# Performance work log

Hardware: AMD Instinct MI355X
Metric: run time of the kernel (lower is better)

## Reference

```python
import jax, jax.numpy as jnp
import numpy as np

B, NB, BS, C, H = 4, 128, 128, 256, 8  # batch, num_blocks, block_size, dim, heads


def setup_inputs() -> dict:
    key = jax.random.key(0)
    ks = jax.random.split(key, 8)
    x = jax.random.normal(ks[0], (B, NB * BS, C), dtype=jnp.float32)
    attn_mask = jax.random.randint(ks[1], (NB, BS, BS + 1), 0, 2, dtype=jnp.int32)
    # guarantee the global-node column is always attendable (avoids all--inf rows)
    attn_mask = attn_mask.at[:, :, BS].set(1)
    edge_feats = jax.random.normal(ks[2], (NB, BS, BS + 1, 4), dtype=jnp.float32)
    w_qkv = jax.random.normal(ks[3], (C, 3 * C), dtype=jnp.float32) * (C ** -0.5)
    b_qkv = jnp.zeros((3 * C,), dtype=jnp.float32)
    w_proj = jax.random.normal(ks[4], (C, C), dtype=jnp.float32) * (C ** -0.5)
    b_proj = jnp.zeros((C,), dtype=jnp.float32)
    w_gate = jax.random.normal(ks[5], (4, H), dtype=jnp.float32) * 0.01  # nn.init.normal_(std=0.01)
    b_gate = jnp.zeros((H,), dtype=jnp.float32)
    return {"x": x, "attn_mask": attn_mask, "edge_feats": edge_feats,
            "w_qkv": w_qkv, "b_qkv": b_qkv, "w_proj": w_proj, "b_proj": b_proj,
            "w_gate": w_gate, "b_gate": b_gate}


def reference(x, attn_mask, edge_feats, w_qkv, b_qkv, w_proj, b_proj, w_gate, b_gate):
    Bv, N, Cv = x.shape
    nb, bs, _ = attn_mask.shape
    Hv = b_gate.shape[0]
    hd = Cv // Hv
    scale = hd ** -0.5

    x_blk = x.reshape(Bv, nb, bs, Cv)
    block_node = x_blk.mean(axis=2, keepdims=True)           # [B, nb, 1, C]
    kv = jnp.concatenate([x_blk, block_node], axis=2)        # [B, nb, bs+1, C]

    qkv_q = x_blk @ w_qkv + b_qkv
    qkv_kv = kv @ w_qkv + b_qkv
    q = qkv_q[..., :Cv].reshape(Bv, nb, bs, Hv, hd)
    k = qkv_kv[..., Cv:2 * Cv].reshape(Bv, nb, bs + 1, Hv, hd)
    v = qkv_kv[..., 2 * Cv:].reshape(Bv, nb, bs + 1, Hv, hd)

    scores = jnp.einsum('bnqhd,bnkhd->bnqkh', q, k) * scale  # [B, nb, bs, bs+1, H]

    # physics bias: zero out (with channel-3 = 1) at the global-node column and the diagonal
    qi = jnp.arange(bs)[:, None]
    ki = jnp.arange(bs + 1)[None, :]
    special = (ki == bs) | (ki == qi)                        # [bs, bs+1]
    special_vec = jnp.array([0.0, 0.0, 0.0, 1.0], dtype=x.dtype)
    bias = jnp.where(special[:, :, None], special_vec, edge_feats[..., :4])  # [nb, bs, bs+1, 4]
    bias = jnp.broadcast_to(bias[None], (Bv, nb, bs, bs + 1, 4))

    scores = scores + bias[..., 3:4]
    mask = (attn_mask[None, :, :, :, None] != 0)             # [1, nb, bs, bs+1, 1]
    scores = jnp.where(mask, scores, -jnp.inf)
    probs = jax.nn.softmax(scores, axis=3)

    gate = jnp.where(mask, bias @ w_gate + b_gate, jnp.zeros((), dtype=x.dtype))
    combined = probs + gate                                  # [B, nb, bs, bs+1, H]

    out = jnp.einsum('bnqkh,bnkhd->bnqhd', combined, v).reshape(Bv, N, Cv)
    return out @ w_proj + b_proj
```

## Files before the change

### kernel.cpp

```cpp
#include <hip/hip_runtime.h>

#define B_   4
#define NB_  128
#define BS_  128
#define C_   256
#define H_   8
#define KL_  129
#define SC2_   0.25503486f
#define LOG2E_ 1.4426950408889634f
#define LN2_   0.6931471805599453f
#define RSTR_  99072

typedef unsigned short u16;
typedef unsigned int   u32;
typedef short          s16;
typedef __attribute__((ext_vector_type(8))) __bf16 bf16x8;
typedef __attribute__((ext_vector_type(4))) float  f32x4;

__device__ __forceinline__ float bf16tof(u16 u) {
  union { u32 i; float f; } v; v.i = ((u32)u) << 16; return v.f;
}
__device__ __forceinline__ u16 ftobf16(float f) {
  union { float f; u32 i; } v; v.f = f;
  u32 b = v.i + 0x7FFFu + ((v.i >> 16) & 1u);
  return (u16)(b >> 16);
}
__device__ __forceinline__ u32 pk2(float a, float b) {
  return (u32)ftobf16(a) | ((u32)ftobf16(b) << 16);
}
__device__ __forceinline__ float asf(u32 u) {
  union { u32 i; float f; } v; v.i = u; return v.f;
}

__device__ __forceinline__ void glds16(const void* g, void* l) {
  __builtin_amdgcn_global_load_lds(
      (const __attribute__((address_space(1))) unsigned int*)g,
      (__attribute__((address_space(3))) unsigned int*)l, 16, 0, 0);
}

__global__ __launch_bounds__(256) void meancvt_kernel(const float* __restrict__ x,
                                                      u16* __restrict__ xb) {
  const int blk = blockIdx.x;
  const int c = threadIdx.x;
  const float* p = x + (size_t)blk * BS_ * C_ + c;
  u16* q = xb + (size_t)blk * (KL_ * C_) + c;
  float s = 0.f;
  #pragma unroll 4
  for (int r = 0; r < BS_; ++r) {
    const float v = p[(size_t)r * C_];
    s += v;
    q[(size_t)r * C_] = ftobf16(v);
  }
  q[(size_t)BS_ * C_] = ftobf16(s * (1.0f / BS_));
}

__global__ __launch_bounds__(256) void wt_kernel(const float* __restrict__ wq,
      const float* __restrict__ wp, s16* __restrict__ wtq, s16* __restrict__ wtp) {
  const int i = blockIdx.x * 256 + threadIdx.x;
  if (i < 768 * 256) {
    const int nn = i >> 8, k = i & 255;
    wtq[i] = (s16)ftobf16(wq[k * 768 + nn]);
  } else {
    const int j = i - 768 * 256;
    const int nn = j >> 8, k = j & 255;
    wtp[j] = (s16)ftobf16(wp[k * 256 + nn]);
  }
}

__global__ __launch_bounds__(256) void pre_kernel(const int* __restrict__ mask,
      const float* __restrict__ ef, u16* __restrict__ e4t) {
  const int t = blockIdx.x * 256 + threadIdx.x;
  const int kq = t & 31;
  const int row = t >> 5;
  const int q = row & 127;
  const int key0 = kq * 4;
  const int* mrow = mask + (size_t)row * KL_;
  const float* erow = ef + (size_t)row * KL_ * 4;
  u32 o[8];
  #pragma unroll
  for (int r = 0; r < 4; ++r) {
    const int key = key0 + r;
    const int m = mrow[key];
    float4 e = *(const float4*)(erow + (size_t)key * 4);
    if (key == q) { e.x = 0.f; e.y = 0.f; e.z = 0.f; e.w = 1.f; }
    float e3L = e.w * LOG2E_;
    if (!m) { e.x = 0.f; e.y = 0.f; e.z = 0.f; e3L = -1e30f; }
    o[2*r]   = (u32)ftobf16(e.x) | ((u32)ftobf16(e.y) << 16);
    o[2*r+1] = (u32)ftobf16(e.z) | ((u32)ftobf16(e3L) << 16);
  }
  uint4* dst = (uint4*)(e4t + (size_t)row * 512 + key0 * 4);
  dst[0] = uint4{o[0], o[1], o[2], o[3]};
  dst[1] = uint4{o[4], o[5], o[6], o[7]};
}

template<bool STRIDED, bool OBF16, int NS>
__global__ __launch_bounds__(256) void mfma_gemm(const s16* __restrict__ Ab,
      const s16* __restrict__ Bt, const float* __restrict__ bias,
      void* __restrict__ outv) {
  __shared__ __align__(16) s16 Al[2][128 * 64];
  __shared__ __align__(16) s16 Bl[2][128 * 64];
  const int tid = threadIdx.x;
  const int lane = tid & 63;
  const int wid = tid >> 6;
  const int row0 = blockIdx.y * 128;
  const int col0 = blockIdx.x * 128;
  const int ldrow = lane >> 3;
  const int lcb   = (lane & 7) * 16;

  auto STAGE = [&](int k0, int buf) {
    #pragma unroll
    for (int j = 0; j < 4; ++j) {
      const int c = wid * 4 + j;
      const int row = c * 8 + ldrow;
      const int scb = lcb ^ ((row & 7) << 4);
      glds16(Bt + (size_t)(col0 + row) * C_ + k0 + (scb >> 1), &Bl[buf][c * 512]);
    }
    #pragma unroll
    for (int j = 0; j < 4; ++j) {
      const int c = wid * 4 + j;
      const int row = c * 8 + ldrow;
      const int scb = lcb ^ ((row & 7) << 4);
      if constexpr (STRIDED)
        glds16(Ab + (size_t)blockIdx.y * RSTR_ + (size_t)row * 768 + 256
                  + k0 + (scb >> 1), &Al[buf][c * 512]);
      else
        glds16(Ab + (size_t)(row0 + row) * C_ + k0 + (scb >> 1), &Al[buf][c * 512]);
    }
  };

  f32x4 acc[4][4];
  #pragma unroll
  for (int i = 0; i < 4; ++i)
    #pragma unroll
    for (int j = 0; j < 4; ++j) acc[i][j] = f32x4{0.f, 0.f, 0.f, 0.f};

  STAGE(0, 0);
  __syncthreads();

  const int fr = lane & 15;
  const int ar0 = (wid >> 1) * 64;
  const int ac0 = (wid & 1) * 64;
  #pragma unroll 1
  for (int t = 0; t < 4; ++t) {
    if (t < 3) STAGE((t + 1) * 64, (t + 1) & 1);
    const char* Ac = (const char*)&Al[t & 1][0];
    const char* Bc = (const char*)&Bl[t & 1][0];
    #pragma unroll
    for (int kk = 0; kk < 64; kk += 32) {
      const int kb = kk * 2 + (lane >> 4) * 16;
      bf16x8 af[4], bfr[4];
      #pragma unroll
      for (int mf = 0; mf < 4; ++mf) {
        const int row = ar0 + mf * 16 + fr;
        af[mf] = *(const bf16x8*)(Ac + row * 128 + (kb ^ ((row & 7) << 4)));
      }
      #pragma unroll
      for (int nf = 0; nf < 4; ++nf) {
        const int row = ac0 + nf * 16 + fr;
        bfr[nf] = *(const bf16x8*)(Bc + row * 128 + (kb ^ ((row & 7) << 4)));
      }
      #pragma unroll
      for (int mf = 0; mf < 4; ++mf)
        #pragma unroll
        for (int nf = 0; nf < 4; ++nf)
          acc[mf][nf] = __builtin_amdgcn_mfma_f32_16x16x32_bf16(
              af[mf], bfr[nf], acc[mf][nf], 0, 0, 0);
    }
    __syncthreads();
  }

  const int orow0 = row0 + (wid >> 1) * 64 + (lane >> 4) * 4;
  const int ocol0 = col0 + (wid & 1) * 64 + (lane & 15);
  #pragma unroll
  for (int nf = 0; nf < 4; ++nf) {
    const int col = ocol0 + nf * 16;
    const float bb = bias[col];
    #pragma unroll
    for (int mf = 0; mf < 4; ++mf) {
      #pragma unroll
      for (int r = 0; r < 4; ++r) {
        const size_t row = (size_t)(orow0 + mf * 16 + r);
        const float v = acc[mf][nf][r] + bb;
        if constexpr (OBF16) ((u16*)outv)[row * NS + col] = ftobf16(v);
        else                 ((float*)outv)[row * NS + col] = v;
      }
    }
  }
}

__global__ __launch_bounds__(256, 4) void attn_kernel(u16* __restrict__ qkv,
      const u16* __restrict__ e4t, const float* __restrict__ wg_,
      const float* __restrict__ bg) {
  __shared__ __align__(16) char lds[36176];
  const int bid = blockIdx.x;
  const int xcd = bid & 7;
  const int j   = bid >> 3;
  const int wgi = xcd * 64 + (j >> 3);
  const int h   = j & 7;
  const int n = wgi & (NB_ - 1);
  const int tid = threadIdx.x;
  const int wid = tid >> 6, lane = tid & 63;
  const int g = lane >> 4, ql = lane & 15;
  u16*  Kl = (u16*)lds;
  u16*  vt = (u16*)(lds + 10320);
  char* pb = lds + 18768 + wid * 4352;

  u16* qkv_blk = qkv + (size_t)wgi * RSTR_;
  const u16* ebase = e4t + (size_t)n * (128 * 512);

  for (int i = tid; i < 516; i += 256) {
    const int r = i >> 2, dc = i & 3;
    const uint4 u = *(const uint4*)(qkv_blk + (size_t)r * 768 + 256 + h * 32 + dc * 8);
    *(uint4*)(Kl + r * 40 + dc * 8) = u;
  }
  for (int i = tid; i < 512; i += 256) {
    const int r = i >> 2, dc = i & 3;
    const uint4 u = *(const uint4*)(qkv_blk + (size_t)r * 768 + 512 + h * 32 + dc * 8);
    u16* col = vt + (dc * 8) * 132 + r;
    col[0 * 132] = (u16)(u.x & 0xffff); col[1 * 132] = (u16)(u.x >> 16);
    col[2 * 132] = (u16)(u.y & 0xffff); col[3 * 132] = (u16)(u.y >> 16);
    col[4 * 132] = (u16)(u.z & 0xffff); col[5 * 132] = (u16)(u.z >> 16);
    col[6 * 132] = (u16)(u.w & 0xffff); col[7 * 132] = (u16)(u.w >> 16);
  }
  __syncthreads();

  const float v128a = bf16tof(qkv_blk[(size_t)128 * 768 + 512 + h * 32 + ql]);
  const float v128b = bf16tof(qkv_blk[(size_t)128 * 768 + 512 + h * 32 + 16 + ql]);

  const float wgc0 = wg_[h], wgc1 = wg_[8 + h], wgc2 = wg_[16 + h];
  const float wgc3s = wg_[24 + h] * LN2_;
  const float bgh = bg[h];
  const float gk128 = wg_[24 + h] + bgh;

  #pragma unroll 1
  for (int mi = 0; mi < 2; ++mi) {
    const int mt = wid * 2 + mi;
    const int qrow = mt * 16 + ql;
    const bf16x8 qf = *(const bf16x8*)(qkv_blk + (size_t)qrow * 768 + h * 32 + g * 8);
    const uint4* eql = (const uint4*)(ebase + (size_t)qrow * 512) + 2 * g;

    float psum = 0.f;
    uint2 gab[8];
    #pragma unroll
    for (int f = 0; f < 8; ++f) {
      const bf16x8 kf = *(const bf16x8*)(Kl + (16 * f + ql) * 40 + 8 * g);
      f32x4 st = __builtin_amdgcn_mfma_f32_16x16x32_bf16(
          kf, qf, f32x4{0.f, 0.f, 0.f, 0.f}, 0, 0, 0);
      const uint4 ea = eql[8 * f];
      const uint4 eb = eql[8 * f + 1];
      const u32 wa[4] = {ea.x, ea.z, eb.x, eb.z};
      const u32 wb[4] = {ea.y, ea.w, eb.y, eb.w};
      float w[4], gt[4];
      #pragma unroll
      for (int r = 0; r < 4; ++r) {
        const float e0 = asf(wa[r] << 16), e1 = asf(wa[r] & 0xffff0000u);
        const float e2 = asf(wb[r] << 16), e3L = asf(wb[r] & 0xffff0000u);
        const float gg = fmaf(e0, wgc0, fmaf(e1, wgc1,
                          fmaf(e2, wgc2, fmaf(e3L, wgc3s, bgh))));
        gt[r] = (e3L > -1e29f) ? gg : 0.f;
        w[r] = __builtin_amdgcn_exp2f(fmaf(st[r], SC2_, e3L));
        psum += w[r];
      }
      gab[f] = uint2{pk2(gt[0], gt[1]), pk2(gt[2], gt[3])};
      *(uint2*)(pb + ql * 272 + (16 * f + 4 * g) * 2) =
          uint2{pk2(w[0], w[1]), pk2(w[2], w[3])};
    }
    const bf16x8 kf8 = *(const bf16x8*)(Kl + 128 * 40 + 8 * g);
    f32x4 st8 = __builtin_amdgcn_mfma_f32_16x16x32_bf16(
        kf8, qf, f32x4{0.f, 0.f, 0.f, 0.f}, 0, 0, 0);
    const float w0 = __builtin_amdgcn_exp2f(
        fmaf(st8[0], SC2_, (g == 0) ? LOG2E_ : -1e30f));
    psum += w0;
    psum += __shfl_xor(psum, 16);
    psum += __shfl_xor(psum, 32);
    const float inv = __builtin_amdgcn_rcpf(psum);
    const float c128 = fmaf(w0, inv, (g == 0) ? gk128 : 0.f);

    f32x4 ow0{0.f,0.f,0.f,0.f}, ow1{0.f,0.f,0.f,0.f};
    #pragma unroll
    for (int c = 0; c < 4; ++c) {
      const bf16x8 pa = *(const bf16x8*)(pb + ql * 272 + (32 * c + 8 * g) * 2);
      const bf16x8 v0 = *(const bf16x8*)(vt + ql * 132 + 32 * c + 8 * g);
      const bf16x8 v1 = *(const bf16x8*)(vt + (16 + ql) * 132 + 32 * c + 8 * g);
      ow0 = __builtin_amdgcn_mfma_f32_16x16x32_bf16(pa, v0, ow0, 0, 0, 0);
      ow1 = __builtin_amdgcn_mfma_f32_16x16x32_bf16(pa, v1, ow1, 0, 0, 0);
    }
    #pragma unroll
    for (int f = 0; f < 8; ++f)
      *(uint2*)(pb + ql * 272 + (16 * f + 4 * g) * 2) = gab[f];
    f32x4 og0{0.f,0.f,0.f,0.f}, og1{0.f,0.f,0.f,0.f};
    #pragma unroll
    for (int c = 0; c < 4; ++c) {
      const bf16x8 pa = *(const bf16x8*)(pb + ql * 272 + (32 * c + 8 * g) * 2);
      const bf16x8 v0 = *(const bf16x8*)(vt + ql * 132 + 32 * c + 8 * g);
      const bf16x8 v1 = *(const bf16x8*)(vt + (16 + ql) * 132 + 32 * c + 8 * g);
      og0 = __builtin_amdgcn_mfma_f32_16x16x32_bf16(pa, v0, og0, 0, 0, 0);
      og1 = __builtin_amdgcn_mfma_f32_16x16x32_bf16(pa, v1, og1, 0, 0, 0);
    }
    u16* aop = qkv_blk + (size_t)(mt * 16 + g * 4) * 768 + 256 + h * 32 + ql;
    #pragma unroll
    for (int r = 0; r < 4; ++r) {
      const float iv = __shfl(inv,  4 * g + r);
      const float cc = __shfl(c128, 4 * g + r);
      aop[(size_t)r * 768]      = ftobf16(fmaf(cc, v128a, fmaf(ow0[r], iv, og0[r])));
      aop[(size_t)r * 768 + 16] = ftobf16(fmaf(cc, v128b, fmaf(ow1[r], iv, og1[r])));
    }
  }
}

extern "C" void kernel_launch(void* const* d_in, const int* in_sizes, int n_in,
                              void* d_out, int out_size, void* d_ws, size_t ws_size,
                              hipStream_t stream) {
  (void)in_sizes; (void)n_in; (void)out_size; (void)ws_size;
  const float* x      = (const float*)d_in[0];
  const int*   mask   = (const int*)  d_in[1];
  const float* ef     = (const float*)d_in[2];
  const float* w_qkv  = (const float*)d_in[3];
  const float* b_qkv  = (const float*)d_in[4];
  const float* w_proj = (const float*)d_in[5];
  const float* b_proj = (const float*)d_in[6];
  const float* w_gate = (const float*)d_in[7];
  const float* b_gate = (const float*)d_in[8];
  float* out = (float*)d_out;
  char* ws = (char*)d_ws;

  u16* qkv = (u16*)(ws);
  s16* wtq = (s16*)(ws + 101449728);
  s16* wtp = (s16*)(ws + 101842944);
  u16* xb  = (u16*)(ws + 101974016);
  u16* e4t = (u16*)(ws + 101974016);

  meancvt_kernel<<<B_ * NB_, 256, 0, stream>>>(x, xb);
  wt_kernel<<<(768 * 256 + 256 * 256) / 256, 256, 0, stream>>>(
      w_qkv, w_proj, wtq, wtp);
  mfma_gemm<false, true, 768>
      <<<dim3(6, (B_ * NB_ * KL_) / 128), 256, 0, stream>>>(
      (const s16*)xb, wtq, b_qkv, qkv);
  pre_kernel<<<(NB_ * BS_ * 32) / 256, 256, 0, stream>>>(mask, ef, e4t);
  attn_kernel<<<B_ * NB_ * H_, 256, 0, stream>>>(
      qkv, (const u16*)e4t, w_gate, b_gate);
  mfma_gemm<true, false, 256>
      <<<dim3(2, (B_ * NB_ * BS_) / 128), 256, 0, stream>>>(
      (const s16*)qkv, wtp, b_proj, out);
}
```

Baseline: 213.0 us.

## Remap GEMM tiles per XCD and use hardware bf16 conversion

The two MFMA GEMMs now launch on a 1D grid, and block indices are remapped so that consecutive tiles sharing the same A rows land on the same XCD (blockIdx & 7 selects a contiguous chunk). This is meant to improve L2 reuse of A and B tiles across the chiplets. Separately, the manual round-to-nearest-even bf16 conversion is replaced with the compiler's __bf16 cast, which may lower to native conversion instructions and cut ALU work. The compiler cast may round NaNs or edge cases slightly differently from the hand-written version.

```diff
diff --git a/kernel.cpp b/kernel.cpp
--- a/kernel.cpp
+++ b/kernel.cpp
@@ -20,13 +20,13 @@
 __device__ __forceinline__ float bf16tof(u16 u) {
   union { u32 i; float f; } v; v.i = ((u32)u) << 16; return v.f;
 }
-__device__ __forceinline__ u16 ftobf16(float f) {
-  union { float f; u32 i; } v; v.f = f;
-  u32 b = v.i + 0x7FFFu + ((v.i >> 16) & 1u);
-  return (u16)(b >> 16);
+__device__ __forceinline__ u16 fbits(float a) {
+  union { __bf16 h; u16 u; } v; v.h = (__bf16)a; return v.u;
 }
 __device__ __forceinline__ u32 pk2(float a, float b) {
-  return (u32)ftobf16(a) | ((u32)ftobf16(b) << 16);
+  union { __bf16 h[2]; u32 u; } v;
+  v.h[0] = (__bf16)a; v.h[1] = (__bf16)b;
+  return v.u;
 }
 __device__ __forceinline__ float asf(u32 u) {
   union { u32 i; float f; } v; v.i = u; return v.f;
@@ -49,9 +49,9 @@
   for (int r = 0; r < BS_; ++r) {
     const float v = p[(size_t)r * C_];
     s += v;
-    q[(size_t)r * C_] = ftobf16(v);
-  }
-  q[(size_t)BS_ * C_] = ftobf16(s * (1.0f / BS_));
+    q[(size_t)r * C_] = fbits(v);
+  }
+  q[(size_t)BS_ * C_] = fbits(s * (1.0f / BS_));
 }
 
 __global__ __launch_bounds__(256) void wt_kernel(const float* __restrict__ wq,
@@ -59,11 +59,11 @@
   const int i = blockIdx.x * 256 + threadIdx.x;
   if (i < 768 * 256) {
     const int nn = i >> 8, k = i & 255;
-    wtq[i] = (s16)ftobf16(wq[k * 768 + nn]);
+    wtq[i] = (s16)fbits(wq[k * 768 + nn]);
   } else {
     const int j = i - 768 * 256;
     const int nn = j >> 8, k = j & 255;
-    wtp[j] = (s16)ftobf16(wp[k * 256 + nn]);
+    wtp[j] = (s16)fbits(wp[k * 256 + nn]);
   }
 }
 
@@ -85,8 +85,8 @@
     if (key == q) { e.x = 0.f; e.y = 0.f; e.z = 0.f; e.w = 1.f; }
     float e3L = e.w * LOG2E_;
     if (!m) { e.x = 0.f; e.y = 0.f; e.z = 0.f; e3L = -1e30f; }
-    o[2*r]   = (u32)ftobf16(e.x) | ((u32)ftobf16(e.y) << 16);
-    o[2*r+1] = (u32)ftobf16(e.z) | ((u32)ftobf16(e3L) << 16);
+    o[2*r]   = pk2(e.x, e.y);
+    o[2*r+1] = pk2(e.z, e3L);
   }
   uint4* dst = (uint4*)(e4t + (size_t)row * 512 + key0 * 4);
   dst[0] = uint4{o[0], o[1], o[2], o[3]};
@@ -102,8 +102,12 @@
   const int tid = threadIdx.x;
   const int lane = tid & 63;
   const int wid = tid >> 6;
-  const int row0 = blockIdx.y * 128;
-  const int col0 = blockIdx.x * 128;
+  constexpr int ncol = NS / 128;
+  const int per  = gridDim.x >> 3;
+  const int gidx = (blockIdx.x & 7) * per + (blockIdx.x >> 3);
+  const int arow = gidx / ncol;
+  const int col0 = (gidx - arow * ncol) * 128;
+  const int row0 = arow * 128;
   const int ldrow = lane >> 3;
   const int lcb   = (lane & 7) * 16;
 
@@ -121,7 +125,7 @@
       const int row = c * 8 + ldrow;
       const int scb = lcb ^ ((row & 7) << 4);
       if constexpr (STRIDED)
-        glds16(Ab + (size_t)blockIdx.y * RSTR_ + (size_t)row * 768 + 256
+        glds16(Ab + (size_t)arow * RSTR_ + (size_t)row * 768 + 256
                   + k0 + (scb >> 1), &Al[buf][c * 512]);
       else
         glds16(Ab + (size_t)(row0 + row) * C_ + k0 + (scb >> 1), &Al[buf][c * 512]);
@@ -181,7 +185,7 @@
       for (int r = 0; r < 4; ++r) {
         const size_t row = (size_t)(orow0 + mf * 16 + r);
         const float v = acc[mf][nf][r] + bb;
-        if constexpr (OBF16) ((u16*)outv)[row * NS + col] = ftobf16(v);
+        if constexpr (OBF16) ((u16*)outv)[row * NS + col] = fbits(v);
         else                 ((float*)outv)[row * NS + col] = v;
       }
     }
@@ -302,8 +306,8 @@
     for (int r = 0; r < 4; ++r) {
       const float iv = __shfl(inv,  4 * g + r);
       const float cc = __shfl(c128, 4 * g + r);
-      aop[(size_t)r * 768]      = ftobf16(fmaf(cc, v128a, fmaf(ow0[r], iv, og0[r])));
-      aop[(size_t)r * 768 + 16] = ftobf16(fmaf(cc, v128b, fmaf(ow1[r], iv, og1[r])));
+      aop[(size_t)r * 768]      = fbits(fmaf(cc, v128a, fmaf(ow0[r], iv, og0[r])));
+      aop[(size_t)r * 768 + 16] = fbits(fmaf(cc, v128b, fmaf(ow1[r], iv, og1[r])));
     }
   }
 }
@@ -334,12 +338,12 @@
   wt_kernel<<<(768 * 256 + 256 * 256) / 256, 256, 0, stream>>>(
       w_qkv, w_proj, wtq, wtp);
   mfma_gemm<false, true, 768>
-      <<<dim3(6, (B_ * NB_ * KL_) / 128), 256, 0, stream>>>(
+      <<<(B_ * NB_ * KL_ / 128) * 6, 256, 0, stream>>>(
       (const s16*)xb, wtq, b_qkv, qkv);
   pre_kernel<<<(NB_ * BS_ * 32) / 256, 256, 0, stream>>>(mask, ef, e4t);
   attn_kernel<<<B_ * NB_ * H_, 256, 0, stream>>>(
       qkv, (const u16*)e4t, w_gate, b_gate);
   mfma_gemm<true, false, 256>
-      <<<dim3(2, (B_ * NB_ * BS_) / 128), 256, 0, stream>>>(
+      <<<(B_ * NB_ * BS_ / 128) * 2, 256, 0, stream>>>(
       (const s16*)qkv, wtp, b_proj, out);
 }
```

Result: faster. 196.8 us (-7.6%).
